# Kernel tuning notes

Hardware: AMD Instinct MI355X
Metric: run time of the kernel (lower is better)

The kernel has to match this reference:

```python
import jax, jax.numpy as jnp
import numpy as np

B, L, D = 2, 2048, 2048
H, HKV, HD = 32, 8, 64
EPS = 1e-5
THETA = 1000000.0


def rms_norm(x, w):
    # normalize over last dim (head_dim)
    return x * jax.lax.rsqrt(jnp.mean(x * x, axis=-1, keepdims=True) + EPS) * w


def apply_rope(t):
    # t: (B, heads, L, HD); non-traditional (half-split) RoPE, offset=0
    half = HD // 2
    inv_freq = THETA ** (-jnp.arange(0, HD, 2, dtype=jnp.float32) / HD)  # (half,)
    ang = jnp.arange(L, dtype=jnp.float32)[:, None] * inv_freq           # (L, half)
    cos, sin = jnp.cos(ang), jnp.sin(ang)
    x1, x2 = t[..., :half], t[..., half:]
    return jnp.concatenate([x1 * cos - x2 * sin, x2 * cos + x1 * sin], axis=-1)


def setup_inputs() -> dict:
    key = jax.random.key(0)
    ks = jax.random.split(key, 5)
    s = 0.02
    return {
        "x": jax.random.normal(ks[0], (B, L, D), dtype=jnp.float32),
        "Wq": jax.random.normal(ks[1], (D, H * HD), dtype=jnp.float32) * s,
        "Wk": jax.random.normal(ks[2], (D, HKV * HD), dtype=jnp.float32) * s,
        "Wv": jax.random.normal(ks[3], (D, HKV * HD), dtype=jnp.float32) * s,
        "Wo": jax.random.normal(ks[4], (H * HD, D), dtype=jnp.float32) * s,
        "q_norm_w": jnp.ones((HD,), dtype=jnp.float32),
        "k_norm_w": jnp.ones((HD,), dtype=jnp.float32),
    }


def reference(x, Wq, Wk, Wv, Wo, q_norm_w, k_norm_w):
    scale = HD ** -0.5
    g = H // HKV  # GQA group size
    # projections
    q = (x @ Wq).reshape(B, L, H, HD)
    k = (x @ Wk).reshape(B, L, HKV, HD)
    v = (x @ Wv).reshape(B, L, HKV, HD)
    # per-head RMSNorm, then to (B, heads, L, HD)
    q = jnp.transpose(rms_norm(q, q_norm_w), (0, 2, 1, 3))
    k = jnp.transpose(rms_norm(k, k_norm_w), (0, 2, 1, 3))
    v = jnp.transpose(v, (0, 2, 1, 3))
    # RoPE
    q = apply_rope(q)
    k = apply_rope(k)
    # grouped-query attention with causal mask
    qg = q.reshape(B, HKV, g, L, HD)
    scores = jnp.einsum('bhgqd,bhkd->bhgqk', qg, k) * scale  # (B,HKV,g,L,L)
    causal = jnp.tril(jnp.ones((L, L), dtype=bool))
    scores = jnp.where(causal, scores, jnp.finfo(scores.dtype).min)
    probs = jax.nn.softmax(scores, axis=-1)
    out = jnp.einsum('bhgqk,bhkd->bhgqd', probs, v)           # (B,HKV,g,L,HD)
    out = jnp.transpose(out.reshape(B, H, L, HD), (0, 2, 1, 3)).reshape(B, L, H * HD)
    return out @ Wo
```

## Files before the change

kernel.cpp:

```cpp
#include <hip/hip_runtime.h>
#include <math.h>
#include <stdint.h>

#define B_ 2
#define L_ 2048
#define D_ 2048
#define H_ 32
#define HKV_ 8
#define HD_ 64
#define EPS_ 1e-5f

typedef _Float16 half_t;
typedef __attribute__((ext_vector_type(8))) _Float16 half8_t;
typedef __attribute__((ext_vector_type(4))) _Float16 half4_t;
typedef __attribute__((ext_vector_type(4))) float float4_t;

typedef const __attribute__((address_space(1))) uint32_t glb_u32;
typedef __attribute__((address_space(3))) uint32_t lds_u32;
#define GLOAD_LDS16(gp, lp) \
  __builtin_amdgcn_global_load_lds((glb_u32*)(gp), (lds_u32*)(lp), 16, 0, 0)

__device__ __forceinline__ float4_t fmax4(float4_t a, float4_t b) {
  float4_t r;
  r[0] = fmaxf(a[0], b[0]); r[1] = fmaxf(a[1], b[1]);
  r[2] = fmaxf(a[2], b[2]); r[3] = fmaxf(a[3], b[3]);
  return r;
}

__device__ __forceinline__ uint32_t pk_f16(float a, float b) {
  auto p = __builtin_amdgcn_cvt_pkrtz(a, b);
  return __builtin_bit_cast(uint32_t, p);
}

__global__ __launch_bounds__(256) void prep_all(
    const float* __restrict__ x,
    const float* __restrict__ Wq, const float* __restrict__ Wk,
    const float* __restrict__ Wv, const float* __restrict__ Wo,
    half_t* __restrict__ xh,
    half_t* __restrict__ Wqt, half_t* __restrict__ Wkt,
    half_t* __restrict__ Wvt, half_t* __restrict__ Wot)
{
  __shared__ float tile[64][65];
  const int t = threadIdx.x;
  int id = blockIdx.x;

  if (id < 4096) {
    size_t i = ((size_t)id * 256 + t) * 8;
    float4 v0 = *(const float4*)&x[i];
    float4 v1 = *(const float4*)&x[i + 4];
    half8_t h;
    h[0] = (half_t)v0.x; h[1] = (half_t)v0.y; h[2] = (half_t)v0.z; h[3] = (half_t)v0.w;
    h[4] = (half_t)v1.x; h[5] = (half_t)v1.y; h[6] = (half_t)v1.z; h[7] = (half_t)v1.w;
    *(half8_t*)&xh[i] = h;
    return;
  }
  id -= 4096;
  const float* W; half_t* Wt; int N;
  if (id < 1024)      { W = Wq; Wt = Wqt; N = 2048; }
  else if (id < 1280) { id -= 1024; W = Wk; Wt = Wkt; N = 512; }
  else if (id < 1536) { id -= 1280; W = Wv; Wt = Wvt; N = 512; }
  else                { id -= 1536; W = Wo; Wt = Wot; N = 2048; }
  const int K = 2048;
  int tk = id & 31, tn = id >> 5;
  int k0 = tk * 64, n0 = tn * 64;

  int rr = t >> 6, cc = t & 63;
#pragma unroll
  for (int i = 0; i < 16; i++)
    tile[rr + i * 4][cc] = W[(size_t)(k0 + rr + i * 4) * N + n0 + cc];
  __syncthreads();

  int rn = t >> 2, q4 = (t & 3) * 16;
  half8_t h0, h1;
#pragma unroll
  for (int u = 0; u < 8; u++) h0[u] = (half_t)tile[q4 + u][rn];
#pragma unroll
  for (int u = 0; u < 8; u++) h1[u] = (half_t)tile[q4 + 8 + u][rn];
  *(half8_t*)&Wt[(size_t)(n0 + rn) * K + k0 + q4]     = h0;
  *(half8_t*)&Wt[(size_t)(n0 + rn) * K + k0 + q4 + 8] = h1;
}

template <typename CT>
__device__ __forceinline__ void gemm_tile_f16(
    const half_t* __restrict__ A, const half_t* __restrict__ Bt,
    CT* __restrict__ C, int K, int ldc, int row0, int col0)
{
  __shared__ __align__(16) half_t As[128 * 32];
  __shared__ __align__(16) half_t Bs[128 * 32];
  const int t    = threadIdx.x;
  const int lane = t & 63;
  const int w    = t >> 6;
  const int quad = lane >> 4, c = lane & 15;
  const int wm = (w >> 1) * 64, wn = (w & 1) * 64;

  float4_t acc[4][4];
#pragma unroll
  for (int i = 0; i < 4; i++)
#pragma unroll
    for (int j = 0; j < 4; j++) acc[i][j] = (float4_t){0.f, 0.f, 0.f, 0.f};

  const int srow = w * 32 + (lane >> 2);
  const int scol = (lane & 3) * 8;
  const half_t* Ag0 = A  + (size_t)(row0 + srow) * K + scol;
  const half_t* Ag1 = Ag0 + (size_t)16 * K;
  const half_t* Bg0 = Bt + (size_t)(col0 + srow) * K + scol;
  const half_t* Bg1 = Bg0 + (size_t)16 * K;
  half_t* As_w0 = &As[(w * 32) * 32];
  half_t* As_w1 = &As[(w * 32 + 16) * 32];
  half_t* Bs_w0 = &Bs[(w * 32) * 32];
  half_t* Bs_w1 = &Bs[(w * 32 + 16) * 32];

  for (int k0 = 0; k0 < K; k0 += 32) {
    __syncthreads();
    GLOAD_LDS16(Ag0 + k0, As_w0);
    GLOAD_LDS16(Ag1 + k0, As_w1);
    GLOAD_LDS16(Bg0 + k0, Bs_w0);
    GLOAD_LDS16(Bg1 + k0, Bs_w1);
    __syncthreads();

    half8_t af[4], bf[4];
#pragma unroll
    for (int i = 0; i < 4; i++)
      af[i] = *(const half8_t*)&As[(wm + i * 16 + c) * 32 + quad * 8];
#pragma unroll
    for (int j = 0; j < 4; j++)
      bf[j] = *(const half8_t*)&Bs[(wn + j * 16 + c) * 32 + quad * 8];
#pragma unroll
    for (int i = 0; i < 4; i++)
#pragma unroll
      for (int j = 0; j < 4; j++)
        acc[i][j] = __builtin_amdgcn_mfma_f32_16x16x32_f16(af[i], bf[j], acc[i][j], 0, 0, 0);
  }

#pragma unroll
  for (int i = 0; i < 4; i++)
#pragma unroll
    for (int r = 0; r < 4; r++) {
      CT* Cp = C + (size_t)(row0 + wm + i * 16 + quad * 4 + r) * ldc + col0 + wn + c;
#pragma unroll
      for (int j = 0; j < 4; j++)
        Cp[j * 16] = (CT)acc[i][j][r];
    }
}

__global__ __launch_bounds__(256) void qkv_gemm_h(
    const half_t* __restrict__ xh,
    const half_t* __restrict__ Wqt, const half_t* __restrict__ Wkt,
    const half_t* __restrict__ Wvt,
    half_t* __restrict__ qh, half_t* __restrict__ kh, half_t* __restrict__ vh)
{
  int bx = blockIdx.x;
  const half_t* Bt; half_t* C; int ldc, col0;
  if (bx < 16)      { Bt = Wqt; C = qh; ldc = H_ * HD_;   col0 = bx * 128; }
  else if (bx < 20) { Bt = Wkt; C = kh; ldc = HKV_ * HD_; col0 = (bx - 16) * 128; }
  else              { Bt = Wvt; C = vh; ldc = HKV_ * HD_; col0 = (bx - 20) * 128; }
  gemm_tile_f16<half_t>(xh, Bt, C, D_, ldc, blockIdx.y * 128, col0);
}

__global__ __launch_bounds__(256) void out_gemm_h(
    const half_t* __restrict__ attn, const half_t* __restrict__ Wot,
    float* __restrict__ out)
{
  gemm_tile_f16<float>(attn, Wot, out, H_ * HD_, D_, blockIdx.y * 128, blockIdx.x * 128);
}

__device__ __forceinline__ void norm_rope_body(
    half_t* buf, const float* w, int wave, int nheads, int lognh,
    int lane, float oscale)
{
  int head  = wave & (nheads - 1);
  int token = wave >> lognh;
  int l     = token & (L_ - 1);

  size_t idx = (size_t)token * (nheads * HD_) + head * HD_ + lane;
  float x = (float)buf[idx];

  float ss = x * x;
#pragma unroll
  for (int off = 32; off; off >>= 1) ss += __shfl_xor(ss, off);
  float xn = x * rsqrtf(ss * (1.0f / HD_) + EPS_) * w[lane];

  float partner = __shfl_xor(xn, 32);
  int   fi = lane & 31;
  float inv_freq = exp2f((float)fi * -0.622862853f);
  float ang = (float)l * inv_freq;
  float cv = cosf(ang), sv = sinf(ang);
  float res = (lane < 32) ? (xn * cv - partner * sv) : (xn * cv + partner * sv);
  buf[idx] = (half_t)(res * oscale);
}

__global__ __launch_bounds__(256) void postproc(
    half_t* __restrict__ qh, half_t* __restrict__ kh,
    const half_t* __restrict__ vh, half_t* __restrict__ vt,
    const float* __restrict__ qw, const float* __restrict__ kw)
{
  const int t = threadIdx.x;
  int id = blockIdx.x;
  if (id < 32768) {
    int wave = id * 4 + (t >> 6);
    norm_rope_body(qh, qw, wave, H_, 5, t & 63, 0.180336880f);
    return;
  }
  id -= 32768;
  if (id < 8192) {
    int wave = id * 4 + (t >> 6);
    norm_rope_body(kh, kw, wave, HKV_, 3, t & 63, 1.0f);
    return;
  }
  id -= 8192;
  int kk0 = (id & 31) * 64, kvh = (id >> 5) & 7, b = id >> 8;
  int d = t >> 2, uu = t & 3;
  const half_t* src = vh + (size_t)(b * L_) * (HKV_ * HD_) + kvh * HD_ + d;
  half_t* dst = vt + ((size_t)((b * HKV_ + kvh) * HD_ + d)) * L_ + kk0 + uu * 16;
  half_t vals[16];
#pragma unroll
  for (int u = 0; u < 16; u++)
    vals[u] = src[(size_t)(kk0 + uu * 16 + u) * (HKV_ * HD_)];
#pragma unroll
  for (int u = 0; u < 16; u += 4)
    *(half4_t*)&dst[u] = *(half4_t*)&vals[u];
}

__global__ __launch_bounds__(512) void flash_mfma2(
    const half_t* __restrict__ Qh, const half_t* __restrict__ Kh,
    const half_t* __restrict__ Vt, half_t* __restrict__ Oa)
{
  __shared__ __align__(16) half_t Ks[64][72];
  __shared__ __align__(16) half_t Vs[64][72];
  __shared__ __align__(16) half_t Ps[128][72];
  __shared__ __align__(16) float  Ab[128];

  const int t    = threadIdx.x;
  const int w    = t >> 6;
  const int lane = t & 63;
  const int quad = lane >> 4;
  const int c    = lane & 15;
  const int h = blockIdx.y, b = blockIdx.z;
  const int kvh = h >> 2;

  const half_t* kbase = Kh + (size_t)(b * L_) * (HKV_ * HD_) + kvh * HD_;
  const half_t* vbase = Vt + (size_t)((b * HKV_ + kvh) * HD_) * L_;
  const int sr = t >> 3;
  const int su = (t & 7) * 8;

  half8_t ones;
#pragma unroll
  for (int u = 0; u < 8; u++) ones[u] = (half_t)1.0f;

  for (int pass = 0; pass < 2; pass++) {
    const int qb  = pass ? (15 - (int)blockIdx.x) : (int)blockIdx.x;
    const int q0  = qb * 128;
    const int wq0 = q0 + w * 16;

    half8_t qf0, qf1;
    {
      const half_t* qp = Qh + ((size_t)(b * L_ + wq0 + c)) * (H_ * HD_) + h * HD_;
      qf0 = *(const half8_t*)&qp[quad * 8];
      qf1 = *(const half8_t*)&qp[32 + quad * 8];
    }

    float4_t o[5];
#pragma unroll
    for (int dt = 0; dt < 5; dt++) o[dt] = (float4_t){0.f, 0.f, 0.f, 0.f};
    float mm = -__builtin_inff();

    half8_t kr, vr;
    kr = *(const half8_t*)(kbase + (size_t)sr * (HKV_ * HD_) + su);
    vr = *(const half8_t*)(vbase + (size_t)sr * L_ + su);

    const int last = (q0 + 127) >> 6;
    for (int kt = 0; kt <= last; kt++) {
      const int kk0 = kt * 64;
      __syncthreads();
      *(half8_t*)&Ks[sr][su] = kr;
      *(half8_t*)&Vs[sr][su] = vr;
      __syncthreads();
      if (kt < last) {
        kr = *(const half8_t*)(kbase + (size_t)(kk0 + 64 + sr) * (HKV_ * HD_) + su);
        vr = *(const half8_t*)(vbase + (size_t)sr * L_ + kk0 + 64 + su);
      }
      if (kk0 > wq0 + 15) continue;

      float4_t S[4];
      __builtin_amdgcn_s_setprio(1);
#pragma unroll
      for (int tt = 0; tt < 4; tt++) {
        half8_t kf0 = *(const half8_t*)&Ks[tt * 16 + c][quad * 8];
        half8_t kf1 = *(const half8_t*)&Ks[tt * 16 + c][32 + quad * 8];
        float4_t s = (float4_t){0.f, 0.f, 0.f, 0.f};
        s = __builtin_amdgcn_mfma_f32_16x16x32_f16(kf0, qf0, s, 0, 0, 0);
        s = __builtin_amdgcn_mfma_f32_16x16x32_f16(kf1, qf1, s, 0, 0, 0);
        S[tt] = s;
      }
      __builtin_amdgcn_s_setprio(0);

      if (kk0 + 63 > wq0) {
#pragma unroll
        for (int tt = 0; tt < 4; tt++) {
          int base = kk0 + tt * 16 + quad * 4 - (wq0 + c);
#pragma unroll
          for (int r = 0; r < 4; r++)
            if (base + r > 0) S[tt][r] = -__builtin_inff();
        }
      }

      {
        float4_t m4 = fmax4(fmax4(S[0], S[1]), fmax4(S[2], S[3]));
        float mloc = fmaxf(fmaxf(m4[0], m4[1]), fmaxf(m4[2], m4[3]));
        mloc = fmaxf(mloc, __shfl_xor(mloc, 16));
        mloc = fmaxf(mloc, __shfl_xor(mloc, 32));
        if (__any(mloc > mm + 8.0f)) {
          float mnew = fmaxf(mm, mloc);
          float al = exp2f(mm - mnew);
          mm = mnew;
          if (quad == 0) Ab[w * 16 + c] = al;
          float4_t av = *(const float4_t*)&Ab[w * 16 + quad * 4];
#pragma unroll
          for (int dt = 0; dt < 5; dt++)
#pragma unroll
            for (int r = 0; r < 4; r++) o[dt][r] *= av[r];
        }
#pragma unroll
        for (int tt = 0; tt < 4; tt++) {
#pragma unroll
          for (int r = 0; r < 4; r++) S[tt][r] = exp2f(S[tt][r] - mm);
          uint2 pw;
          pw.x = pk_f16(S[tt][0], S[tt][1]);
          pw.y = pk_f16(S[tt][2], S[tt][3]);
          *(uint2*)&Ps[w * 16 + c][tt * 16 + quad * 4] = pw;
        }
      }

      half8_t pf0 = *(const half8_t*)&Ps[w * 16 + c][quad * 8];
      half8_t pf1 = *(const half8_t*)&Ps[w * 16 + c][32 + quad * 8];
      __builtin_amdgcn_s_setprio(1);
      o[4] = __builtin_amdgcn_mfma_f32_16x16x32_f16(pf0, ones, o[4], 0, 0, 0);
      o[4] = __builtin_amdgcn_mfma_f32_16x16x32_f16(pf1, ones, o[4], 0, 0, 0);
#pragma unroll
      for (int dt = 0; dt < 4; dt++) {
        half8_t vf0 = *(const half8_t*)&Vs[dt * 16 + c][quad * 8];
        half8_t vf1 = *(const half8_t*)&Vs[dt * 16 + c][32 + quad * 8];
        o[dt] = __builtin_amdgcn_mfma_f32_16x16x32_f16(pf0, vf0, o[dt], 0, 0, 0);
        o[dt] = __builtin_amdgcn_mfma_f32_16x16x32_f16(pf1, vf1, o[dt], 0, 0, 0);
      }
      __builtin_amdgcn_s_setprio(0);
    }

#pragma unroll
    for (int r = 0; r < 4; r++) {
      float inv = 1.0f / o[4][r];
      half_t* op = Oa + ((size_t)(b * L_ + wq0 + quad * 4 + r)) * (H_ * HD_)
                 + h * HD_ + c;
#pragma unroll
      for (int dt = 0; dt < 4; dt++)
        op[dt * 16] = (half_t)(o[dt][r] * inv);
    }
  }
}

extern "C" void kernel_launch(void* const* d_in, const int* in_sizes, int n_in,
                              void* d_out, int out_size, void* d_ws, size_t ws_size,
                              hipStream_t stream)
{
  const float* x  = (const float*)d_in[0];
  const float* Wq = (const float*)d_in[1];
  const float* Wk = (const float*)d_in[2];
  const float* Wv = (const float*)d_in[3];
  const float* Wo = (const float*)d_in[4];
  const float* qw = (const float*)d_in[5];
  const float* kw = (const float*)d_in[6];
  float* out = (float*)d_out;

  const size_t XN = (size_t)B_ * L_ * D_;
  const size_t QN = (size_t)B_ * L_ * H_ * HD_;
  const size_t KN = (size_t)B_ * L_ * HKV_ * HD_;
  const size_t WQ = (size_t)D_ * H_ * HD_;
  const size_t WK = (size_t)D_ * HKV_ * HD_;

  half_t* p   = (half_t*)d_ws;
  half_t* xh  = p;  p += XN;
  half_t* Wqt = p;  p += WQ;
  half_t* Wkt = p;  p += WK;
  half_t* Wvt = p;  p += WK;
  half_t* Wot = p;  p += WQ;
  half_t* qh  = p;  p += QN;
  half_t* kh  = p;  p += KN;
  half_t* vh  = p;  p += KN;
  half_t* vt  = p;  p += KN;
  half_t* attn = xh;

  prep_all<<<6656, 256, 0, stream>>>(x, Wq, Wk, Wv, Wo, xh, Wqt, Wkt, Wvt, Wot);

  qkv_gemm_h<<<dim3(24, 32), 256, 0, stream>>>(xh, Wqt, Wkt, Wvt, qh, kh, vh);

  postproc<<<32768 + 8192 + 512, 256, 0, stream>>>(qh, kh, vh, vt, qw, kw);

  flash_mfma2<<<dim3(8, H_, B_), 512, 0, stream>>>(qh, kh, vt, attn);

  out_gemm_h<<<dim3(16, 32), 256, 0, stream>>>(attn, Wot, out);
}
```

Measured before the change: 335.5 us.

## Fuse QK RMSNorm and RoPE into QKV GEMM epilogue with trig table

```diff
diff --git a/kernel.cpp b/kernel.cpp
--- a/kernel.cpp
+++ b/kernel.cpp
@@ -80,18 +80,31 @@
   *(half8_t*)&Wt[(size_t)(n0 + rn) * K + k0 + q4 + 8] = h1;
 }
 
+__global__ __launch_bounds__(256) void build_trig(
+    float* __restrict__ ct, float* __restrict__ st)
+{
+  int e = blockIdx.x * 256 + threadIdx.x;
+  int l = e >> 5, fi = e & 31;
+  float inv_freq = exp2f((float)fi * -0.622862853f);
+  float ang = (float)l * inv_freq;
+  ct[e] = cosf(ang);
+  st[e] = sinf(ang);
+}
+
 template <typename CT>
 __device__ __forceinline__ void gemm_tile_f16(
     const half_t* __restrict__ A, const half_t* __restrict__ Bt,
-    CT* __restrict__ C, int K, int ldc, int row0, int col0)
+    CT* __restrict__ C, int K, int ldc, int row0, int col0,
+    bool donorm, const float* __restrict__ w,
+    const float* __restrict__ ct, const float* __restrict__ st, float oscale)
 {
   __shared__ __align__(16) half_t As[128 * 32];
   __shared__ __align__(16) half_t Bs[128 * 32];
   const int t    = threadIdx.x;
   const int lane = t & 63;
-  const int w    = t >> 6;
+  const int w4   = t >> 6;
   const int quad = lane >> 4, c = lane & 15;
-  const int wm = (w >> 1) * 64, wn = (w & 1) * 64;
+  const int wm = (w4 >> 1) * 64, wn = (w4 & 1) * 64;
 
   float4_t acc[4][4];
 #pragma unroll
@@ -99,16 +112,16 @@
 #pragma unroll
     for (int j = 0; j < 4; j++) acc[i][j] = (float4_t){0.f, 0.f, 0.f, 0.f};
 
-  const int srow = w * 32 + (lane >> 2);
+  const int srow = w4 * 32 + (lane >> 2);
   const int scol = (lane & 3) * 8;
   const half_t* Ag0 = A  + (size_t)(row0 + srow) * K + scol;
   const half_t* Ag1 = Ag0 + (size_t)16 * K;
   const half_t* Bg0 = Bt + (size_t)(col0 + srow) * K + scol;
   const half_t* Bg1 = Bg0 + (size_t)16 * K;
-  half_t* As_w0 = &As[(w * 32) * 32];
-  half_t* As_w1 = &As[(w * 32 + 16) * 32];
-  half_t* Bs_w0 = &Bs[(w * 32) * 32];
-  half_t* Bs_w1 = &Bs[(w * 32 + 16) * 32];
+  half_t* As_w0 = &As[(w4 * 32) * 32];
+  half_t* As_w1 = &As[(w4 * 32 + 16) * 32];
+  half_t* Bs_w0 = &Bs[(w4 * 32) * 32];
+  half_t* Bs_w1 = &Bs[(w4 * 32 + 16) * 32];
 
   for (int k0 = 0; k0 < K; k0 += 32) {
     __syncthreads();
@@ -132,82 +145,91 @@
         acc[i][j] = __builtin_amdgcn_mfma_f32_16x16x32_f16(af[i], bf[j], acc[i][j], 0, 0, 0);
   }
 
-#pragma unroll
-  for (int i = 0; i < 4; i++)
-#pragma unroll
-    for (int r = 0; r < 4; r++) {
-      CT* Cp = C + (size_t)(row0 + wm + i * 16 + quad * 4 + r) * ldc + col0 + wn + c;
-#pragma unroll
-      for (int j = 0; j < 4; j++)
-        Cp[j * 16] = (CT)acc[i][j][r];
-    }
+  if (donorm) {
+    float w0 = w[c], w1 = w[16 + c], w2 = w[32 + c], w3 = w[48 + c];
+#pragma unroll
+    for (int i = 0; i < 4; i++)
+#pragma unroll
+      for (int r = 0; r < 4; r++) {
+        int row = row0 + wm + i * 16 + quad * 4 + r;
+        float a0 = acc[i][0][r], a1 = acc[i][1][r];
+        float a2 = acc[i][2][r], a3 = acc[i][3][r];
+        float ss = a0 * a0 + a1 * a1 + a2 * a2 + a3 * a3;
+        ss += __shfl_xor(ss, 1);
+        ss += __shfl_xor(ss, 2);
+        ss += __shfl_xor(ss, 4);
+        ss += __shfl_xor(ss, 8);
+        float rn = rsqrtf(ss * (1.0f / HD_) + EPS_);
+        float x0 = a0 * rn * w0, x1 = a1 * rn * w1;
+        float x2 = a2 * rn * w2, x3 = a3 * rn * w3;
+        int l = row & (L_ - 1);
+        float cv0 = ct[l * 32 + c],      sv0 = st[l * 32 + c];
+        float cv1 = ct[l * 32 + 16 + c], sv1 = st[l * 32 + 16 + c];
+        float r0 = x0 * cv0 - x2 * sv0;
+        float r1 = x1 * cv1 - x3 * sv1;
+        float r2 = x2 * cv0 + x0 * sv0;
+        float r3 = x3 * cv1 + x1 * sv1;
+        CT* Cp = C + (size_t)row * ldc + col0 + wn + c;
+        Cp[0]  = (CT)(r0 * oscale);
+        Cp[16] = (CT)(r1 * oscale);
+        Cp[32] = (CT)(r2 * oscale);
+        Cp[48] = (CT)(r3 * oscale);
+      }
+  } else {
+#pragma unroll
+    for (int i = 0; i < 4; i++)
+#pragma unroll
+      for (int r = 0; r < 4; r++) {
+        CT* Cp = C + (size_t)(row0 + wm + i * 16 + quad * 4 + r) * ldc + col0 + wn + c;
+#pragma unroll
+        for (int j = 0; j < 4; j++)
+          Cp[j * 16] = (CT)acc[i][j][r];
+      }
+  }
 }
 
 __global__ __launch_bounds__(256) void qkv_gemm_h(
     const half_t* __restrict__ xh,
     const half_t* __restrict__ Wqt, const half_t* __restrict__ Wkt,
     const half_t* __restrict__ Wvt,
-    half_t* __restrict__ qh, half_t* __restrict__ kh, half_t* __restrict__ vh)
-{
-  int bx = blockIdx.x;
+    half_t* __restrict__ qh, half_t* __restrict__ kh, half_t* __restrict__ vh,
+    const float* __restrict__ qw, const float* __restrict__ kw,
+    const float* __restrict__ ct, const float* __restrict__ st)
+{
+  int lin = (int)blockIdx.y * 24 + (int)blockIdx.x;
+  int xcd = lin & 7, idx = lin >> 3;
+  int cy = xcd >> 2, cx = xcd & 3;
+  int by = cy * 16 + idx / 6;
+  int bx = cx * 6 + idx % 6;
+
   const half_t* Bt; half_t* C; int ldc, col0;
+  bool donorm = true; const float* w = qw; float osc = 0.180336880f;
   if (bx < 16)      { Bt = Wqt; C = qh; ldc = H_ * HD_;   col0 = bx * 128; }
-  else if (bx < 20) { Bt = Wkt; C = kh; ldc = HKV_ * HD_; col0 = (bx - 16) * 128; }
-  else              { Bt = Wvt; C = vh; ldc = HKV_ * HD_; col0 = (bx - 20) * 128; }
-  gemm_tile_f16<half_t>(xh, Bt, C, D_, ldc, blockIdx.y * 128, col0);
+  else if (bx < 20) { Bt = Wkt; C = kh; ldc = HKV_ * HD_; col0 = (bx - 16) * 128;
+                      w = kw; osc = 1.0f; }
+  else              { Bt = Wvt; C = vh; ldc = HKV_ * HD_; col0 = (bx - 20) * 128;
+                      donorm = false; }
+  gemm_tile_f16<half_t>(xh, Bt, C, D_, ldc, by * 128, col0, donorm, w, ct, st, osc);
 }
 
 __global__ __launch_bounds__(256) void out_gemm_h(
     const half_t* __restrict__ attn, const half_t* __restrict__ Wot,
     float* __restrict__ out)
 {
-  gemm_tile_f16<float>(attn, Wot, out, H_ * HD_, D_, blockIdx.y * 128, blockIdx.x * 128);
-}
-
-__device__ __forceinline__ void norm_rope_body(
-    half_t* buf, const float* w, int wave, int nheads, int lognh,
-    int lane, float oscale)
-{
-  int head  = wave & (nheads - 1);
-  int token = wave >> lognh;
-  int l     = token & (L_ - 1);
-
-  size_t idx = (size_t)token * (nheads * HD_) + head * HD_ + lane;
-  float x = (float)buf[idx];
-
-  float ss = x * x;
-#pragma unroll
-  for (int off = 32; off; off >>= 1) ss += __shfl_xor(ss, off);
-  float xn = x * rsqrtf(ss * (1.0f / HD_) + EPS_) * w[lane];
-
-  float partner = __shfl_xor(xn, 32);
-  int   fi = lane & 31;
-  float inv_freq = exp2f((float)fi * -0.622862853f);
-  float ang = (float)l * inv_freq;
-  float cv = cosf(ang), sv = sinf(ang);
-  float res = (lane < 32) ? (xn * cv - partner * sv) : (xn * cv + partner * sv);
-  buf[idx] = (half_t)(res * oscale);
-}
-
-__global__ __launch_bounds__(256) void postproc(
-    half_t* __restrict__ qh, half_t* __restrict__ kh,
-    const half_t* __restrict__ vh, half_t* __restrict__ vt,
-    const float* __restrict__ qw, const float* __restrict__ kw)
+  int lin = (int)blockIdx.y * 16 + (int)blockIdx.x;
+  int xcd = lin & 7, idx = lin >> 3;
+  int cy = xcd >> 1, cx = xcd & 1;
+  int by = cy * 8 + idx / 8;
+  int bx = cx * 8 + idx % 8;
+  gemm_tile_f16<float>(attn, Wot, out, H_ * HD_, D_, by * 128, bx * 128,
+                       false, nullptr, nullptr, nullptr, 1.0f);
+}
+
+__global__ __launch_bounds__(256) void postproc_v(
+    const half_t* __restrict__ vh, half_t* __restrict__ vt)
 {
   const int t = threadIdx.x;
   int id = blockIdx.x;
-  if (id < 32768) {
-    int wave = id * 4 + (t >> 6);
-    norm_rope_body(qh, qw, wave, H_, 5, t & 63, 0.180336880f);
-    return;
-  }
-  id -= 32768;
-  if (id < 8192) {
-    int wave = id * 4 + (t >> 6);
-    norm_rope_body(kh, kw, wave, HKV_, 3, t & 63, 1.0f);
-    return;
-  }
-  id -= 8192;
   int kk0 = (id & 31) * 64, kvh = (id >> 5) & 7, b = id >> 8;
   int d = t >> 2, uu = t & 3;
   const half_t* src = vh + (size_t)(b * L_) * (HKV_ * HD_) + kvh * HD_ + d;
@@ -389,11 +411,17 @@
   half_t* vt  = p;  p += KN;
   half_t* attn = xh;
 
+  float* ct = (float*)vt;
+  float* st = ct + 65536;
+
   prep_all<<<6656, 256, 0, stream>>>(x, Wq, Wk, Wv, Wo, xh, Wqt, Wkt, Wvt, Wot);
 
-  qkv_gemm_h<<<dim3(24, 32), 256, 0, stream>>>(xh, Wqt, Wkt, Wvt, qh, kh, vh);
-
-  postproc<<<32768 + 8192 + 512, 256, 0, stream>>>(qh, kh, vh, vt, qw, kw);
+  build_trig<<<256, 256, 0, stream>>>(ct, st);
+
+  qkv_gemm_h<<<dim3(24, 32), 256, 0, stream>>>(xh, Wqt, Wkt, Wvt, qh, kh, vh,
+                                               qw, kw, ct, st);
+
+  postproc_v<<<512, 256, 0, stream>>>(vh, vt);
 
   flash_mfma2<<<dim3(8, H_, B_), 512, 0, stream>>>(qh, kh, vt, attn);
 
```

New measurement: 337.0 us. Within noise of the previous version (+0.4%).
